# Kernel tuning notes

Hardware: AMD Instinct MI355X
Metric: run time of the kernel (lower is better)

Reference implementation:

```python
import jax, jax.numpy as jnp
import numpy as np

B, C, H, W = 4, 192, 128, 128
K = 2048            # selected (changed) tokens per image
HEADS = 3
HD = C // HEADS     # 64
HID = 4 * C         # 768, ConvMlp hidden
N = H * W
EPS = 1e-5


def _layernorm(x, w, b):
    mu = jnp.mean(x, axis=-1, keepdims=True)
    var = jnp.mean((x - mu) ** 2, axis=-1, keepdims=True)
    return (x - mu) / jnp.sqrt(var + EPS) * w + b


def setup_inputs() -> dict:
    key = jax.random.key(0)
    ks = jax.random.split(key, 12)
    x = jax.random.normal(ks[0], (B, C, H, W), dtype=jnp.float32)
    # unique sorted indices per batch (scatter-back must be well defined)
    pkeys = jax.random.split(ks[1], B)
    indices = jnp.sort(
        jax.vmap(lambda k: jax.random.permutation(k, N)[:K])(pkeys), axis=-1
    ).astype(jnp.int64)
    s = 0.02
    return {
        "x": x,
        "indices": indices,
        "ln1_w": jnp.ones((C,), jnp.float32),
        "ln1_b": jnp.zeros((C,), jnp.float32),
        "qkv_w": jax.random.normal(ks[2], (3 * C, C), jnp.float32) * s,
        "proj_w": jax.random.normal(ks[3], (C, C), jnp.float32) * s,
        "proj_b": jnp.zeros((C,), jnp.float32),
        "ln2_w": jnp.ones((C,), jnp.float32),
        "ln2_b": jnp.zeros((C,), jnp.float32),
        "fc1_w": jax.random.normal(ks[4], (HID, C), jnp.float32) * s,
        "fc1_b": jnp.zeros((HID,), jnp.float32),
        "dw_w": jax.random.normal(ks[5], (HID, 1, 3, 3), jnp.float32) * s,  # depthwise OIHW
        "fc2_w": jax.random.normal(ks[6], (C, HID), jnp.float32) * s,
        "fc2_b": jnp.zeros((C,), jnp.float32),
    }


def reference(x, indices, ln1_w, ln1_b, qkv_w, proj_w, proj_b,
              ln2_w, ln2_b, fc1_w, fc1_b, dw_w, fc2_w, fc2_b):
    scale = HD ** (-0.5)
    tokens = x.reshape(B, C, N).transpose(0, 2, 1)          # b n c
    y = _layernorm(tokens, ln1_w, ln1_b)

    # --- masked_attn: gather -> dense MHA on subset -> scatter back ---
    br = jnp.arange(B)[:, None]
    sel = y[br, indices]                                    # b k c
    qkv = sel @ qkv_w.T                                     # b k 3c (no bias)
    qkv = qkv.reshape(B, K, 3, HEADS, HD).transpose(2, 0, 3, 1, 4)
    q, k, v = qkv[0], qkv[1], qkv[2]                        # b h k d
    attn = jax.nn.softmax(jnp.einsum("bhqd,bhkd->bhqk", q, k) * scale, axis=-1)
    out = jnp.einsum("bhqk,bhkd->bhqd", attn, v)            # b h k d
    out = out.transpose(0, 2, 1, 3).reshape(B, K, C) @ proj_w.T + proj_b
    y = y.at[br, indices].set(out)

    tokens = tokens + y                                     # residual adds norm1(x) w/ attn-updated subset
    tokens = _layernorm(tokens, ln2_w, ln2_b)

    # --- ConvMlp: fc1 -> depthwise 3x3 -> GELU -> fc2 ---
    h1 = tokens @ fc1_w.T + fc1_b                           # b n hid
    img = h1.transpose(0, 2, 1).reshape(B, HID, H, W)
    img = jax.lax.conv_general_dilated(
        img, dw_w, (1, 1), "SAME",
        dimension_numbers=("NCHW", "OIHW", "NCHW"),
        feature_group_count=HID)
    h1 = img.reshape(B, HID, N).transpose(0, 2, 1)
    h1 = jax.nn.gelu(h1, approximate=False)
    h2 = h1 @ fc2_w.T + fc2_b

    tokens = tokens + h2
    return tokens.transpose(0, 2, 1).reshape(B, C, H, W)
```

## Files before the change

kernel.cpp:

```cpp
#include <hip/hip_runtime.h>

#define B_ 4
#define C_ 192
#define H_ 128
#define W_ 128
#define N_ (H_*W_)
#define K_ 2048
#define HEADS_ 3
#define HD_ 64
#define HID_ 768
#define NC_ 8
#define KC_ (K_/NC_)

typedef __attribute__((ext_vector_type(4))) float f32x4;
typedef __attribute__((ext_vector_type(8))) short bf16x8;

__device__ __forceinline__ unsigned short f2bf(float f){
  unsigned int u = __float_as_uint(f);
  u += 0x7FFFu + ((u >> 16) & 1u);
  return (unsigned short)(u >> 16);
}
__device__ __forceinline__ float bf2f(unsigned short s){
  return __uint_as_float(((unsigned int)s) << 16);
}
__device__ __forceinline__ unsigned cvtpk(float lo, float hi){
  unsigned r;
  asm("v_cvt_pk_bf16_f32 %0, %1, %2" : "=v"(r) : "v"(lo), "v"(hi));
  return r;
}
__device__ __forceinline__ float gelu_fast(float x){
  float y = 0.7978845608f*x*(1.f + 0.044715f*x*x);
  float e = __expf(2.f*fabsf(y));
  float t = 1.f - 2.f/(1.f + e);
  t = copysignf(t, y);
  return 0.5f*x*(1.f + t);
}

__device__ __forceinline__ int load_idx(const unsigned* __restrict__ ip, int pos){
  bool is64 = (ip[1]==0u) & (ip[3]==0u) & (ip[5]==0u) & (ip[7]==0u);
  int v = is64 ? (int)ip[2*pos] : (int)ip[pos];
  return min(max(v, 0), N_-1);
}

__global__ __launch_bounds__(256) void k_ln1(const float* __restrict__ x,
    const float* __restrict__ w, const float* __restrict__ bias,
    unsigned short* __restrict__ y, int b_off){
  int blk = blockIdx.x;
  int bl = blk >> 8;
  int b  = b_off + bl;
  int n0 = (blk & 255) * 64;
  int t  = threadIdx.x;
  int tok = t & 63, q = t >> 6;
  __shared__ float tile[64][C_+1];
  __shared__ float red[8][64];
  __shared__ float wls[C_], bls[C_];
  if (t < C_){ wls[t] = w[t]; bls[t] = bias[t]; }
  const float* xb = x + (size_t)b*C_*N_ + n0;
  float sum = 0.f, sq = 0.f;
#pragma unroll
  for (int i = 0; i < 48; ++i){
    int c = q + 4*i;
    float v = xb[(size_t)c*N_ + tok];
    tile[tok][c] = v;
    sum += v; sq += v*v;
  }
  red[q][tok] = sum; red[4+q][tok] = sq;
  __syncthreads();
  if (q == 0){
    float s  = red[0][tok]+red[1][tok]+red[2][tok]+red[3][tok];
    float s2 = red[4][tok]+red[5][tok]+red[6][tok]+red[7][tok];
    float mu = s*(1.f/C_);
    float rstd = rsqrtf(s2*(1.f/C_) - mu*mu + 1e-5f);
    red[0][tok] = mu; red[1][tok] = rstd;
  }
  __syncthreads();
  unsigned* yb = reinterpret_cast<unsigned*>(y + ((size_t)bl*N_ + n0)*C_);
#pragma unroll
  for (int i = 0; i < 24; ++i){
    int li = t + 256*i;
    int tk = li / 96, c2 = li % 96;
    int c = 2*c2;
    float v0 = (tile[tk][c]  -red[0][tk])*red[1][tk]*wls[c]   + bls[c];
    float v1 = (tile[tk][c+1]-red[0][tk])*red[1][tk]*wls[c+1] + bls[c+1];
    yb[li] = (unsigned)f2bf(v0) | ((unsigned)f2bf(v1) << 16);
  }
}

__global__ __launch_bounds__(256) void k_qkv(const unsigned short* __restrict__ y,
    const unsigned* __restrict__ idx, const float* __restrict__ wq,
    unsigned short* __restrict__ qkv, int b_off){
  const int NT = (3*C_)/64;
  int bid = blockIdx.x;
  int bl  = bid / (16*NT);
  int rem = bid % (16*NT);
  int m0  = (rem / NT) * 128;
  int n0  = (rem % NT) * 64;
  int t = threadIdx.x, lane = t & 63;
  int wv = t >> 6, wm = wv & 1, wn = wv >> 1;
  __shared__ unsigned short Al[128][40];
  __shared__ unsigned short Bl[64][40];
  __shared__ int rows[128];
  if (t < 128) rows[t] = load_idx(idx, (b_off+bl)*K_ + m0 + t);
  __syncthreads();
  f32x4 acc[4][2] = {};
  int l15 = lane & 15, lhi = lane >> 4;
  for (int k0 = 0; k0 < C_; k0 += 32){
    {
      int m = t >> 1;
      const unsigned short* src = y + ((size_t)bl*N_ + rows[m])*C_ + k0;
#pragma unroll
      for (int i = 0; i < 4; ++i){
        int kq = (t & 1) + 2*i;
        *reinterpret_cast<ushort4*>(&Al[m][4*kq]) =
            *reinterpret_cast<const ushort4*>(src + 4*kq);
      }
      int n = t >> 2;
      const float* bsrc = wq + (size_t)(n0+n)*C_ + k0;
#pragma unroll
      for (int i = 0; i < 2; ++i){
        int q = (t & 3) + 4*i;
        float4 v = *reinterpret_cast<const float4*>(bsrc + 4*q);
        ushort4 p; p.x=f2bf(v.x); p.y=f2bf(v.y); p.z=f2bf(v.z); p.w=f2bf(v.w);
        *reinterpret_cast<ushort4*>(&Bl[n][4*q]) = p;
      }
    }
    __syncthreads();
    bf16x8 af[4], bfr[2];
#pragma unroll
    for (int mf = 0; mf < 4; ++mf)
      af[mf] = *reinterpret_cast<const bf16x8*>(&Al[wm*64 + mf*16 + l15][lhi*8]);
#pragma unroll
    for (int nf = 0; nf < 2; ++nf)
      bfr[nf] = *reinterpret_cast<const bf16x8*>(&Bl[wn*32 + nf*16 + l15][lhi*8]);
#pragma unroll
    for (int mf = 0; mf < 4; ++mf)
#pragma unroll
      for (int nf = 0; nf < 2; ++nf)
        acc[mf][nf] = __builtin_amdgcn_mfma_f32_16x16x32_bf16(af[mf], bfr[nf], acc[mf][nf], 0,0,0);
    __syncthreads();
  }
#pragma unroll
  for (int mf = 0; mf < 4; ++mf){
    int mb = m0 + wm*64 + mf*16 + lhi*4;
#pragma unroll
    for (int nf = 0; nf < 2; ++nf){
      int n = n0 + wn*32 + nf*16 + l15;
#pragma unroll
      for (int r = 0; r < 4; ++r)
        qkv[((size_t)bl*K_ + mb + r)*(3*C_) + n] = f2bf(acc[mf][nf][r]);
    }
  }
}

__global__ __launch_bounds__(256) void k_attn(const unsigned short* __restrict__ qkv,
    float* __restrict__ po, float* __restrict__ pml, int nb){
  int bid = blockIdx.x;
  int c   = bid & (NC_-1);
  int qt  = (bid >> 3) & 31;
  int bh  = bid >> 8;
  int h = bh % HEADS_, bl = bh / HEADS_;
  int q0 = qt*64;
  int t = threadIdx.x, lane = t & 63, wv = t >> 6;
  int l15 = lane & 15, lhi = lane >> 4;
  const unsigned short* base = qkv + (size_t)bl*K_*(3*C_) + h*HD_;
  __shared__ unsigned short Ql[64][72];
  __shared__ unsigned short Kl[64][72];
  __shared__ unsigned short Vt[64][72];
  __shared__ unsigned short Pl[4][16][72];
  {
    int r = t >> 2, d0 = (t & 3) * 16;
    const uint4* src = reinterpret_cast<const uint4*>(base + (size_t)(q0+r)*(3*C_) + d0);
    *reinterpret_cast<uint4*>(&Ql[r][d0])   = src[0];
    *reinterpret_cast<uint4*>(&Ql[r][d0+8]) = src[1];
  }
  __syncthreads();
  float m_q = -1e30f, l_q = 0.f;
  f32x4 o[4] = {};
  for (int kt0 = c*KC_; kt0 < c*KC_ + KC_; kt0 += 64){
    {
      int r = t >> 2, d0 = (t & 3) * 16;
      const uint4* src = reinterpret_cast<const uint4*>(base + (size_t)(kt0+r)*(3*C_) + C_ + d0);
      *reinterpret_cast<uint4*>(&Kl[r][d0])   = src[0];
      *reinterpret_cast<uint4*>(&Kl[r][d0+8]) = src[1];
      int kp = t & 31, vd0 = (t >> 5) * 8, k = 2*kp;
      const ushort4* v0 = reinterpret_cast<const ushort4*>(base + (size_t)(kt0+k)*(3*C_)   + 2*C_ + vd0);
      const ushort4* v1 = reinterpret_cast<const ushort4*>(base + (size_t)(kt0+k+1)*(3*C_) + 2*C_ + vd0);
      ushort4 a0 = v0[0], a1 = v0[1], b0 = v1[0], b1 = v1[1];
      unsigned short va[8] = {a0.x,a0.y,a0.z,a0.w,a1.x,a1.y,a1.z,a1.w};
      unsigned short vb[8] = {b0.x,b0.y,b0.z,b0.w,b1.x,b1.y,b1.z,b1.w};
#pragma unroll
      for (int j = 0; j < 8; ++j){
        unsigned u = (unsigned)va[j] | ((unsigned)vb[j] << 16);
        *reinterpret_cast<unsigned*>(&Vt[vd0+j][k]) = u;
      }
    }
    __syncthreads();
    f32x4 s[4] = {};
    __builtin_amdgcn_s_setprio(1);
#pragma unroll
    for (int kt = 0; kt < 2; ++kt){
      bf16x8 qf = *reinterpret_cast<const bf16x8*>(&Ql[wv*16 + l15][kt*32 + lhi*8]);
#pragma unroll
      for (int nt = 0; nt < 4; ++nt){
        bf16x8 kf = *reinterpret_cast<const bf16x8*>(&Kl[nt*16 + l15][kt*32 + lhi*8]);
        s[nt] = __builtin_amdgcn_mfma_f32_16x16x32_bf16(kf, qf, s[nt], 0,0,0);
      }
    }
    __builtin_amdgcn_s_setprio(0);
    float mx = s[0][0];
#pragma unroll
    for (int nt = 0; nt < 4; ++nt)
#pragma unroll
      for (int reg = 0; reg < 4; ++reg) mx = fmaxf(mx, s[nt][reg]);
    mx = fmaxf(mx, __shfl_xor(mx, 16));
    mx = fmaxf(mx, __shfl_xor(mx, 32));
    mx *= 0.125f;
    bool skip = __all(mx <= m_q + 8.f);
    if (!skip){
      float mn = fmaxf(m_q, mx);
      float corr = __expf(m_q - mn);
      l_q *= corr;
      float cr[4];
#pragma unroll
      for (int reg = 0; reg < 4; ++reg) cr[reg] = __shfl(corr, lhi*4 + reg);
#pragma unroll
      for (int nt = 0; nt < 4; ++nt)
#pragma unroll
        for (int reg = 0; reg < 4; ++reg) o[nt][reg] *= cr[reg];
      m_q = mn;
    }
    float ls = 0.f;
#pragma unroll
    for (int nt = 0; nt < 4; ++nt){
      float p0 = __expf(fmaf(s[nt][0], 0.125f, -m_q));
      float p1 = __expf(fmaf(s[nt][1], 0.125f, -m_q));
      float p2 = __expf(fmaf(s[nt][2], 0.125f, -m_q));
      float p3 = __expf(fmaf(s[nt][3], 0.125f, -m_q));
      ls += (p0 + p1) + (p2 + p3);
      uint2 uu;
      uu.x = cvtpk(p0, p1);
      uu.y = cvtpk(p2, p3);
      *reinterpret_cast<uint2*>(&Pl[wv][l15][nt*16 + lhi*4]) = uu;
    }
    ls += __shfl_xor(ls, 16);
    ls += __shfl_xor(ls, 32);
    l_q += ls;
    __threadfence_block();
    __builtin_amdgcn_s_setprio(1);
#pragma unroll
    for (int kt = 0; kt < 2; ++kt){
      bf16x8 pa = *reinterpret_cast<const bf16x8*>(&Pl[wv][l15][kt*32 + lhi*8]);
#pragma unroll
      for (int nt = 0; nt < 4; ++nt){
        bf16x8 vb = *reinterpret_cast<const bf16x8*>(&Vt[nt*16 + l15][kt*32 + lhi*8]);
        o[nt] = __builtin_amdgcn_mfma_f32_16x16x32_bf16(pa, vb, o[nt], 0,0,0);
      }
    }
    __builtin_amdgcn_s_setprio(0);
    __syncthreads();
  }
  int R = nb*HEADS_*K_;
  int rowb = (bl*HEADS_ + h)*K_;
#pragma unroll
  for (int reg = 0; reg < 4; ++reg){
    int rq = rowb + q0 + wv*16 + lhi*4 + reg;
#pragma unroll
    for (int nt = 0; nt < 4; ++nt)
      po[((size_t)c*R + rq)*HD_ + nt*16 + l15] = o[nt][reg];
  }
  if (lhi == 0){
    int rq = rowb + q0 + wv*16 + l15;
    *reinterpret_cast<float2*>(pml + 2*((size_t)c*R + rq)) = make_float2(m_q, l_q);
  }
}

__global__ __launch_bounds__(256) void k_amerge(const float* __restrict__ po,
    const float* __restrict__ pml, unsigned short* __restrict__ ao, int nb){
  int R = nb*HEADS_*K_;
  int row = blockIdx.x*4 + (threadIdx.x >> 6);
  int lane = threadIdx.x & 63;
  float m[NC_], l[NC_];
#pragma unroll
  for (int cc = 0; cc < NC_; ++cc){
    float2 v = *reinterpret_cast<const float2*>(pml + 2*((size_t)cc*R + row));
    m[cc] = v.x; l[cc] = v.y;
  }
  float M = m[0];
#pragma unroll
  for (int cc = 1; cc < NC_; ++cc) M = fmaxf(M, m[cc]);
  float L = 0.f, o = 0.f;
#pragma unroll
  for (int cc = 0; cc < NC_; ++cc){
    float e = __expf(m[cc] - M);
    L += l[cc]*e;
    o += e * po[((size_t)cc*R + row)*HD_ + lane];
  }
  o /= L;
  int q = row & (K_-1);
  int bh = row >> 11;
  int h = bh % HEADS_, bl = bh / HEADS_;
  ao[((size_t)bl*K_ + q)*C_ + h*HD_ + lane] = f2bf(o);
}

__global__ __launch_bounds__(256) void k_proj(const unsigned short* __restrict__ ain,
    const unsigned* __restrict__ idx, const float* __restrict__ pw,
    const float* __restrict__ pb, unsigned short* __restrict__ y, int b_off){
  const int NT = C_/64;
  int bid = blockIdx.x;
  int bl  = bid / (16*NT);
  int rem = bid % (16*NT);
  int m0  = (rem / NT) * 128;
  int n0  = (rem % NT) * 64;
  int t = threadIdx.x, lane = t & 63;
  int wv = t >> 6, wm = wv & 1, wn = wv >> 1;
  __shared__ unsigned short Al[128][40];
  __shared__ unsigned short Bl[64][40];
  __shared__ int rows[128];
  if (t < 128) rows[t] = load_idx(idx, (b_off+bl)*K_ + m0 + t);
  __syncthreads();
  f32x4 acc[4][2] = {};
  int l15 = lane & 15, lhi = lane >> 4;
  for (int k0 = 0; k0 < C_; k0 += 32){
    {
      int m = t >> 1;
      const unsigned short* src = ain + ((size_t)bl*K_ + m0 + m)*C_ + k0;
#pragma unroll
      for (int i = 0; i < 4; ++i){
        int kq = (t & 1) + 2*i;
        *reinterpret_cast<ushort4*>(&Al[m][4*kq]) =
            *reinterpret_cast<const ushort4*>(src + 4*kq);
      }
      int n = t >> 2;
      const float* bsrc = pw + (size_t)(n0+n)*C_ + k0;
#pragma unroll
      for (int i = 0; i < 2; ++i){
        int q = (t & 3) + 4*i;
        float4 v = *reinterpret_cast<const float4*>(bsrc + 4*q);
        ushort4 p; p.x=f2bf(v.x); p.y=f2bf(v.y); p.z=f2bf(v.z); p.w=f2bf(v.w);
        *reinterpret_cast<ushort4*>(&Bl[n][4*q]) = p;
      }
    }
    __syncthreads();
    bf16x8 af[4], bfr[2];
#pragma unroll
    for (int mf = 0; mf < 4; ++mf)
      af[mf] = *reinterpret_cast<const bf16x8*>(&Al[wm*64 + mf*16 + l15][lhi*8]);
#pragma unroll
    for (int nf = 0; nf < 2; ++nf)
      bfr[nf] = *reinterpret_cast<const bf16x8*>(&Bl[wn*32 + nf*16 + l15][lhi*8]);
#pragma unroll
    for (int mf = 0; mf < 4; ++mf)
#pragma unroll
      for (int nf = 0; nf < 2; ++nf)
        acc[mf][nf] = __builtin_amdgcn_mfma_f32_16x16x32_bf16(af[mf], bfr[nf], acc[mf][nf], 0,0,0);
    __syncthreads();
  }
#pragma unroll
  for (int mf = 0; mf < 4; ++mf){
    int mb = wm*64 + mf*16 + lhi*4;
#pragma unroll
    for (int nf = 0; nf < 2; ++nf){
      int n = n0 + wn*32 + nf*16 + l15;
      float bv = pb[n];
#pragma unroll
      for (int r = 0; r < 4; ++r)
        y[((size_t)bl*N_ + rows[mb + r])*C_ + n] = f2bf(acc[mf][nf][r] + bv);
    }
  }
}

__global__ __launch_bounds__(256) void k_ln2(const float* __restrict__ x,
    const unsigned short* __restrict__ y, const float* __restrict__ w,
    const float* __restrict__ bias, float* __restrict__ ln2t, int b_off){
  int blk = blockIdx.x;
  int bl = blk >> 8;
  int b  = b_off + bl;
  int n0 = (blk & 255) * 64;
  int t  = threadIdx.x;
  int tok = t & 63, q = t >> 6;
  __shared__ float tile[64][C_+1];
  __shared__ float red[8][64];
  __shared__ float wls[C_], bls[C_];
  if (t < C_){ wls[t] = w[t]; bls[t] = bias[t]; }
  const unsigned* yb = reinterpret_cast<const unsigned*>(y + ((size_t)bl*N_ + n0)*C_);
#pragma unroll
  for (int i = 0; i < 24; ++i){
    int li = t + 256*i;
    unsigned u = yb[li];
    int tk = li / 96, c2 = li % 96;
    tile[tk][2*c2]   = bf2f((unsigned short)(u & 0xffffu));
    tile[tk][2*c2+1] = bf2f((unsigned short)(u >> 16));
  }
  __syncthreads();
  const float* xb = x + (size_t)b*C_*N_ + n0;
  float sum = 0.f, sq = 0.f;
#pragma unroll
  for (int i = 0; i < 48; ++i){
    int c = q + 4*i;
    float v = xb[(size_t)c*N_ + tok] + tile[tok][c];
    tile[tok][c] = v;
    sum += v; sq += v*v;
  }
  red[q][tok] = sum; red[4+q][tok] = sq;
  __syncthreads();
  if (q == 0){
    float s  = red[0][tok]+red[1][tok]+red[2][tok]+red[3][tok];
    float s2 = red[4][tok]+red[5][tok]+red[6][tok]+red[7][tok];
    float mu = s*(1.f/C_);
    float rstd = rsqrtf(s2*(1.f/C_) - mu*mu + 1e-5f);
    red[0][tok] = mu; red[1][tok] = rstd;
  }
  __syncthreads();
  float* ob = ln2t + (size_t)b*C_*N_ + n0;
  float mu = red[0][tok], rstd = red[1][tok];
#pragma unroll
  for (int i = 0; i < 48; ++i){
    int c = q + 4*i;
    ob[(size_t)c*N_ + tok] = (tile[tok][c]-mu)*rstd*wls[c] + bls[c];
  }
}

__global__ __launch_bounds__(256) void k_fc1(const float* __restrict__ ln2t,
    const float* __restrict__ wgt, const float* __restrict__ bias,
    unsigned short* __restrict__ h1, int b_off){
  int bid = blockIdx.x;
  int bl  = bid >> 8;
  int rem = bid & 255;
  int m0  = (rem >> 1) * 128;
  int nh  = (rem & 1) * 6;
  int t = threadIdx.x, lane = t & 63;
  int wv = t >> 6, wm = wv & 1, wn = wv >> 1;
  int l15 = lane & 15, lhi = lane >> 4;
  __shared__ unsigned short Al[128][200];
  __shared__ unsigned short Bl[64][200];
  const float* a = ln2t + (size_t)(b_off+bl)*C_*N_ + m0;
  unsigned short* hb = h1 + (size_t)bl*HID_*N_;
  {
    int m = t & 127, half = t >> 7;
#pragma unroll
    for (int i = 0; i < 48; ++i){
      int p = half + 2*i;
      float v0 = a[(size_t)(2*p)*N_ + m];
      float v1 = a[(size_t)(2*p+1)*N_ + m];
      unsigned u = (unsigned)f2bf(v0) | ((unsigned)f2bf(v1) << 16);
      *reinterpret_cast<unsigned*>(&Al[m][2*p]) = u;
    }
  }
  for (int nt = 0; nt < 6; ++nt){
    int n0 = (nh + nt)*64;
    __syncthreads();
    {
      int n = t >> 2;
      const float* bsrc = wgt + (size_t)(n0+n)*C_;
#pragma unroll
      for (int i = 0; i < 12; ++i){
        int q = (t & 3) + 4*i;
        float4 v = *reinterpret_cast<const float4*>(bsrc + 4*q);
        ushort4 p; p.x=f2bf(v.x); p.y=f2bf(v.y); p.z=f2bf(v.z); p.w=f2bf(v.w);
        *reinterpret_cast<ushort4*>(&Bl[n][4*q]) = p;
      }
    }
    __syncthreads();
    f32x4 acc[4][2] = {};
#pragma unroll
    for (int ks = 0; ks < 6; ++ks){
      bf16x8 af[4], bfr[2];
#pragma unroll
      for (int mf = 0; mf < 4; ++mf)
        af[mf] = *reinterpret_cast<const bf16x8*>(&Al[wm*64 + mf*16 + l15][ks*32 + lhi*8]);
#pragma unroll
      for (int nf = 0; nf < 2; ++nf)
        bfr[nf] = *reinterpret_cast<const bf16x8*>(&Bl[wn*32 + nf*16 + l15][ks*32 + lhi*8]);
#pragma unroll
      for (int mf = 0; mf < 4; ++mf)
#pragma unroll
        for (int nf = 0; nf < 2; ++nf)
          acc[mf][nf] = __builtin_amdgcn_mfma_f32_16x16x32_bf16(af[mf], bfr[nf], acc[mf][nf], 0,0,0);
    }
#pragma unroll
    for (int mf = 0; mf < 4; ++mf){
      int mb = m0 + wm*64 + mf*16 + lhi*4;
#pragma unroll
      for (int nf = 0; nf < 2; ++nf){
        int n = n0 + wn*32 + nf*16 + l15;
        float bv = bias[n];
        ushort4 pk;
        pk.x = f2bf(acc[mf][nf][0] + bv);
        pk.y = f2bf(acc[mf][nf][1] + bv);
        pk.z = f2bf(acc[mf][nf][2] + bv);
        pk.w = f2bf(acc[mf][nf][3] + bv);
        *reinterpret_cast<ushort4*>(&hb[(size_t)n*N_ + mb]) = pk;
      }
    }
  }
}

__global__ __launch_bounds__(512) void k_fc2f(const unsigned short* __restrict__ h1,
    const float* __restrict__ dw, const float* __restrict__ wgt,
    const float* __restrict__ bias, float* __restrict__ out, int b_off){
  int nwg = gridDim.x;
  int cpx = nwg >> 3;
  int bid = (blockIdx.x & 7)*cpx + (blockIdx.x >> 3);
  int bl  = bid >> 7;
  int r   = bid & 127;
  int b   = b_off + bl;
  int t = threadIdx.x, lane = t & 63, wv = t >> 6;
  int wm = wv & 1, wn = wv >> 1;
  int l15 = lane & 15, lhi = lane >> 4;
  __shared__ unsigned short Ht[2][32][3][136];
  __shared__ unsigned short Alc[128][40];
  __shared__ unsigned short Bl[192][40];
  __shared__ float Dwl[2][288];
  const unsigned short* h1b = h1 + (size_t)bl*HID_*N_;
  f32x4 acc[4][3] = {};
  int cch = t & 31, j0 = (t >> 5) * 8;
  const unsigned short* gp[3]; unsigned short* lp[3]; bool gok[3];
#pragma unroll
  for (int i = 0; i < 3; ++i){
    int li = t + 512*i;
    int ch = li / 48, rm = li % 48, dy = rm >> 4, seg = rm & 15;
    int rr = r - 1 + dy;
    gok[i] = (rr >= 0 && rr < H_);
    gp[i] = h1b + (size_t)ch*N_ + (gok[i] ? rr : 0)*W_ + seg*8;
    lp[i] = &Ht[0][ch][dy][seg*8];
  }
  const float* wgp[3]; unsigned short* blp[3];
#pragma unroll
  for (int i = 0; i < 3; ++i){
    int row = (t >> 3) + 64*i, seg = t & 7;
    wgp[i] = wgt + (size_t)row*HID_ + seg*4;
    blp[i] = &Bl[row][seg*4];
  }
  const float* dgp = dw + t;
  const int HTB = 32*3*136;
  uint4 hr[3]; float4 wr[3]; float dr = 0.f;
  auto hload = [&](){
#pragma unroll
    for (int i = 0; i < 3; ++i)
      hr[i] = gok[i] ? *reinterpret_cast<const uint4*>(gp[i]) : make_uint4(0u,0u,0u,0u);
#pragma unroll
    for (int i = 0; i < 3; ++i) gp[i] += 32*N_;
  };
  auto wload = [&](){
#pragma unroll
    for (int i = 0; i < 3; ++i){ wr[i] = *reinterpret_cast<const float4*>(wgp[i]); wgp[i] += 32; }
  };
  auto dload = [&](){ if (t < 288){ dr = *dgp; dgp += 288; } };
  hload();
#pragma unroll
  for (int i = 0; i < 3; ++i) *reinterpret_cast<uint4*>(lp[i]) = hr[i];
  dload();
  if (t < 288) Dwl[0][t] = dr;
  wload();
  hload(); dload();
  for (int c24 = 0; c24 < 24; ++c24){
    int cur = c24 & 1;
    __syncthreads();
#pragma unroll
    for (int i = 0; i < 3; ++i){
      float4 v = wr[i];
      ushort4 p; p.x=f2bf(v.x); p.y=f2bf(v.y); p.z=f2bf(v.z); p.w=f2bf(v.w);
      *reinterpret_cast<ushort4*>(blp[i]) = p;
    }
    if (c24 < 23) wload();
    {
      const unsigned short* hp = &Ht[0][cch][0][j0] + cur*HTB;
      const float* wp = &Dwl[cur][cch*9];
      float s[8] = {0.f,0.f,0.f,0.f,0.f,0.f,0.f,0.f};
#pragma unroll
      for (int dy = 0; dy < 3; ++dy){
        const unsigned short* rp = hp + dy*136;
        bf16x8 mid = *reinterpret_cast<const bf16x8*>(rp);
        float v[10];
        v[0] = (j0 > 0)   ? bf2f(rp[-1]) : 0.f;
        v[9] = (j0 < 120) ? bf2f(rp[8])  : 0.f;
#pragma unroll
        for (int j = 0; j < 8; ++j) v[1+j] = bf2f((unsigned short)mid[j]);
        float wa = wp[3*dy], wb = wp[3*dy+1], wc = wp[3*dy+2];
#pragma unroll
        for (int j = 0; j < 8; ++j)
          s[j] += v[j]*wa + v[j+1]*wb + v[j+2]*wc;
      }
#pragma unroll
      for (int j = 0; j < 8; ++j)
        Alc[j0+j][cch] = f2bf(gelu_fast(s[j]));
    }
    __syncthreads();
    if (c24 < 23){
      int nxt = cur ^ 1;
#pragma unroll
      for (int i = 0; i < 3; ++i)
        *reinterpret_cast<uint4*>(lp[i] + nxt*HTB) = hr[i];
      if (t < 288) Dwl[nxt][t] = dr;
      if (c24 < 22){ hload(); dload(); }
    }
    bf16x8 af[4], bfr[3];
#pragma unroll
    for (int mf = 0; mf < 4; ++mf)
      af[mf] = *reinterpret_cast<const bf16x8*>(&Alc[wm*64 + mf*16 + l15][lhi*8]);
#pragma unroll
    for (int nf = 0; nf < 3; ++nf)
      bfr[nf] = *reinterpret_cast<const bf16x8*>(&Bl[wn*48 + nf*16 + l15][lhi*8]);
    __builtin_amdgcn_s_setprio(1);
#pragma unroll
    for (int mf = 0; mf < 4; ++mf)
#pragma unroll
      for (int nf = 0; nf < 3; ++nf)
        acc[mf][nf] = __builtin_amdgcn_mfma_f32_16x16x32_bf16(af[mf], bfr[nf], acc[mf][nf], 0,0,0);
    __builtin_amdgcn_s_setprio(0);
  }
#pragma unroll
  for (int mf = 0; mf < 4; ++mf){
    int tok = r*W_ + wm*64 + mf*16 + lhi*4;
#pragma unroll
    for (int nf = 0; nf < 3; ++nf){
      int oc = wn*48 + nf*16 + l15;
      float bv = bias[oc];
      size_t off = ((size_t)b*C_ + oc)*N_ + tok;
      float4 rr = *reinterpret_cast<const float4*>(out + off);
      float4 v = make_float4(rr.x + acc[mf][nf][0] + bv, rr.y + acc[mf][nf][1] + bv,
                             rr.z + acc[mf][nf][2] + bv, rr.w + acc[mf][nf][3] + bv);
      *reinterpret_cast<float4*>(out + off) = v;
    }
  }
}

extern "C" void kernel_launch(void* const* d_in, const int* in_sizes, int n_in,
                              void* d_out, int out_size, void* d_ws, size_t ws_size,
                              hipStream_t stream) {
  const float*    x      = (const float*)d_in[0];
  const unsigned* idx    = (const unsigned*)d_in[1];
  const float*    ln1_w  = (const float*)d_in[2];
  const float*    ln1_b  = (const float*)d_in[3];
  const float*    qkv_w  = (const float*)d_in[4];
  const float*    proj_w = (const float*)d_in[5];
  const float*    proj_b = (const float*)d_in[6];
  const float*    ln2_w  = (const float*)d_in[7];
  const float*    ln2_b  = (const float*)d_in[8];
  const float*    fc1_w  = (const float*)d_in[9];
  const float*    fc1_b  = (const float*)d_in[10];
  const float*    dw_w   = (const float*)d_in[11];
  const float*    fc2_w  = (const float*)d_in[12];
  const float*    fc2_b  = (const float*)d_in[13];
  float* out = (float*)d_out;

  const size_t SZY = (size_t)N_*C_*2;
  const size_t SZQ = (size_t)K_*3*C_*2;
  const size_t SZA = (size_t)K_*C_*2;
  const size_t SZO = (size_t)NC_*HEADS_*K_*HD_*4;
  const size_t SZH = (size_t)HID_*N_*2;
  int nb = (ws_size >= (size_t)B_*SZH) ? B_ : 1;

  char* ws = (char*)d_ws;
  unsigned short* y16  = (unsigned short*)ws;
  unsigned short* qkvb = (unsigned short*)(ws + (size_t)nb*SZY);
  unsigned short* aob  = (unsigned short*)(ws + (size_t)nb*(SZY+SZQ));
  float*          po   = (float*)(ws + (size_t)nb*(SZY+SZQ+SZA));
  float*          pml  = (float*)(ws + (size_t)nb*(SZY+SZQ+SZA+SZO));
  unsigned short* h1s  = (unsigned short*)ws;

  for (int b0 = 0; b0 < B_; b0 += nb){
    k_ln1   <<<nb*256,             256, 0, stream>>>(x, ln1_w, ln1_b, y16, b0);
    k_qkv   <<<nb*16*9,            256, 0, stream>>>(y16, idx, qkv_w, qkvb, b0);
    k_attn  <<<nb*HEADS_*32*NC_,   256, 0, stream>>>(qkvb, po, pml, nb);
    k_amerge<<<nb*HEADS_*K_/4,     256, 0, stream>>>(po, pml, aob, nb);
    k_proj  <<<nb*16*3,            256, 0, stream>>>(aob, idx, proj_w, proj_b, y16, b0);
    k_ln2   <<<nb*256,             256, 0, stream>>>(x, y16, ln2_w, ln2_b, out, b0);
    k_fc1   <<<nb*256,             256, 0, stream>>>(out, fc1_w, fc1_b, h1s, b0);
    k_fc2f  <<<nb*128,             512, 0, stream>>>(h1s, dw_w, fc2_w, fc2_b, out, b0);
  }
}
```

Before: 257.9 us.

## Single-buffer fc2 halo tile, read weights directly, simplify GELU tanh

In the fused depthwise-conv + GELU + fc2 kernel, the double-buffered LDS halo tile and depthwise-weight tile are replaced by one buffer. The depthwise weights are now read per thread from global memory, and the fc2 weight register prefetch is dropped in favour of loads inside the loop. This cuts LDS per block roughly from 80 KB to 51 KB, which may let more 512-thread blocks share a CU, but it exposes global-load latency that the prefetch used to hide. The GELU tanh approximation also loses its fabs/copysign, computing exp(2y) directly; this stays correct because overflow saturates to the right limit.

```diff
diff --git a/kernel.cpp b/kernel.cpp
--- a/kernel.cpp
+++ b/kernel.cpp
@@ -30,9 +30,8 @@
 }
 __device__ __forceinline__ float gelu_fast(float x){
   float y = 0.7978845608f*x*(1.f + 0.044715f*x*x);
-  float e = __expf(2.f*fabsf(y));
+  float e = __expf(2.f*y);
   float t = 1.f - 2.f/(1.f + e);
-  t = copysignf(t, y);
   return 0.5f*x*(1.f + t);
 }
 
@@ -507,10 +506,9 @@
   int t = threadIdx.x, lane = t & 63, wv = t >> 6;
   int wm = wv & 1, wn = wv >> 1;
   int l15 = lane & 15, lhi = lane >> 4;
-  __shared__ unsigned short Ht[2][32][3][136];
+  __shared__ unsigned short Ht[32][3][136];
   __shared__ unsigned short Alc[128][40];
   __shared__ unsigned short Bl[192][40];
-  __shared__ float Dwl[2][288];
   const unsigned short* h1b = h1 + (size_t)bl*HID_*N_;
   f32x4 acc[4][3] = {};
   int cch = t & 31, j0 = (t >> 5) * 8;
@@ -522,7 +520,7 @@
     int rr = r - 1 + dy;
     gok[i] = (rr >= 0 && rr < H_);
     gp[i] = h1b + (size_t)ch*N_ + (gok[i] ? rr : 0)*W_ + seg*8;
-    lp[i] = &Ht[0][ch][dy][seg*8];
+    lp[i] = &Ht[ch][dy][seg*8];
   }
   const float* wgp[3]; unsigned short* blp[3];
 #pragma unroll
@@ -531,9 +529,8 @@
     wgp[i] = wgt + (size_t)row*HID_ + seg*4;
     blp[i] = &Bl[row][seg*4];
   }
-  const float* dgp = dw + t;
-  const int HTB = 32*3*136;
-  uint4 hr[3]; float4 wr[3]; float dr = 0.f;
+  const float* dwp = dw + (size_t)cch*9;
+  uint4 hr[3];
   auto hload = [&](){
 #pragma unroll
     for (int i = 0; i < 3; ++i)
@@ -541,31 +538,25 @@
 #pragma unroll
     for (int i = 0; i < 3; ++i) gp[i] += 32*N_;
   };
-  auto wload = [&](){
-#pragma unroll
-    for (int i = 0; i < 3; ++i){ wr[i] = *reinterpret_cast<const float4*>(wgp[i]); wgp[i] += 32; }
-  };
-  auto dload = [&](){ if (t < 288){ dr = *dgp; dgp += 288; } };
   hload();
 #pragma unroll
   for (int i = 0; i < 3; ++i) *reinterpret_cast<uint4*>(lp[i]) = hr[i];
-  dload();
-  if (t < 288) Dwl[0][t] = dr;
-  wload();
-  hload(); dload();
+  hload();
   for (int c24 = 0; c24 < 24; ++c24){
-    int cur = c24 & 1;
     __syncthreads();
 #pragma unroll
     for (int i = 0; i < 3; ++i){
-      float4 v = wr[i];
+      float4 v = *reinterpret_cast<const float4*>(wgp[i]);
+      wgp[i] += 32;
       ushort4 p; p.x=f2bf(v.x); p.y=f2bf(v.y); p.z=f2bf(v.z); p.w=f2bf(v.w);
       *reinterpret_cast<ushort4*>(blp[i]) = p;
     }
-    if (c24 < 23) wload();
     {
-      const unsigned short* hp = &Ht[0][cch][0][j0] + cur*HTB;
-      const float* wp = &Dwl[cur][cch*9];
+      float w9[9];
+#pragma unroll
+      for (int i = 0; i < 9; ++i) w9[i] = dwp[i];
+      dwp += 288;
+      const unsigned short* hp = &Ht[cch][0][j0];
       float s[8] = {0.f,0.f,0.f,0.f,0.f,0.f,0.f,0.f};
 #pragma unroll
       for (int dy = 0; dy < 3; ++dy){
@@ -576,7 +567,7 @@
         v[9] = (j0 < 120) ? bf2f(rp[8])  : 0.f;
 #pragma unroll
         for (int j = 0; j < 8; ++j) v[1+j] = bf2f((unsigned short)mid[j]);
-        float wa = wp[3*dy], wb = wp[3*dy+1], wc = wp[3*dy+2];
+        float wa = w9[3*dy], wb = w9[3*dy+1], wc = w9[3*dy+2];
 #pragma unroll
         for (int j = 0; j < 8; ++j)
           s[j] += v[j]*wa + v[j+1]*wb + v[j+2]*wc;
@@ -587,12 +578,10 @@
     }
     __syncthreads();
     if (c24 < 23){
-      int nxt = cur ^ 1;
 #pragma unroll
       for (int i = 0; i < 3; ++i)
-        *reinterpret_cast<uint4*>(lp[i] + nxt*HTB) = hr[i];
-      if (t < 288) Dwl[nxt][t] = dr;
-      if (c24 < 22){ hload(); dload(); }
+        *reinterpret_cast<uint4*>(lp[i]) = hr[i];
+      if (c24 < 22) hload();
     }
     bf16x8 af[4], bfr[3];
 #pragma unroll
```

Result: no change. 256.3 us (-0.6%).
